# Kernel tuning notes

Measured on AMD Instinct MI355X. Metric: run time of the kernel, lower is better.

## Reference

```python
import jax, jax.numpy as jnp
import numpy as np

H = W = 96                      # image_size (scaled down from (240,240) for working-set control)
K = 16                          # faces_per_pixel
SIGMA = 1e-4
GAMMA = 1e-4
BLUR = float(np.log(1.0 / 1e-4 - 1.0) * SIGMA)   # blur_radius, compared against squared NDC dist (pytorch3d convention)
ZNEAR, ZFAR = 1.0, 100.0        # softmax_rgb_blend defaults
EPS = 1e-10


def _edge_d2(p, a, b):
    # squared point-to-segment distance; p:[B,P,F,2], a,b:[B,1,F,2]
    ab = b - a
    ap = p - a
    t = jnp.clip((ap * ab).sum(-1) / ((ab * ab).sum(-1) + 1e-12), 0.0, 1.0)
    d = ap - t[..., None] * ab
    return (d * d).sum(-1)


def _render(meshes_positions, meshes_rotations, meshes_scale, cam_pos, cam_rot, vertices, vert_colors, faces_packed):
    B, M, _ = meshes_positions.shape
    V = vertices.shape[1]
    # per-mesh scale -> rotate -> translate (forward of MeshesRenderer)
    scaled = meshes_scale[:, :, None, :] * vertices[None]                           # [B,M,V,3]
    world = jnp.einsum('bmij,bmvj->bmvi', meshes_rotations, scaled) + meshes_positions[:, :, None, :]
    world = world.reshape(B, M * V, 3)
    # pytorch3d camera: X_cam = X_world @ R + T
    cam = jnp.einsum('bvj,bji->bvi', world, cam_rot) + cam_pos[:, None, :]
    z = cam[..., 2]                                                                 # [B,N]
    xy = cam[..., :2] / z[..., None]                                                # perspective, focal=1 (NDC)

    tri = xy[:, faces_packed]                                                       # [B,F,3,2]
    tz = z[:, faces_packed]                                                         # [B,F,3]
    fcol = vert_colors.reshape(M * V, 3)[faces_packed]                              # [F,3,3]

    xs = (jnp.arange(W, dtype=xy.dtype) + 0.5) * 2.0 / W - 1.0
    ys = 1.0 - (jnp.arange(H, dtype=xy.dtype) + 0.5) * 2.0 / H
    gx, gy = jnp.meshgrid(xs, ys)
    pix = jnp.stack([gx.ravel(), gy.ravel()], -1)[None, :, None, :]                 # [1,P,1,2]

    v0 = tri[:, None, :, 0]; v1 = tri[:, None, :, 1]; v2 = tri[:, None, :, 2]       # [B,1,F,2]
    e1 = v1 - v0; e2 = v2 - v0
    d = pix - v0                                                                    # [B,P,F,2]
    den = e1[..., 0] * e2[..., 1] - e1[..., 1] * e2[..., 0] + 1e-12
    b1 = (d[..., 0] * e2[..., 1] - d[..., 1] * e2[..., 0]) / den                    # barycentrics [B,P,F]
    b2 = (e1[..., 0] * d[..., 1] - e1[..., 1] * d[..., 0]) / den
    b0 = 1.0 - b1 - b2
    zpix = b0 * tz[:, None, :, 0] + b1 * tz[:, None, :, 1] + b2 * tz[:, None, :, 2]
    inside = (b0 >= 0) & (b1 >= 0) & (b2 >= 0)
    d2 = jnp.minimum(jnp.minimum(_edge_d2(pix, v0, v1), _edge_d2(pix, v1, v2)), _edge_d2(pix, v2, v0))
    dists = jnp.where(inside, -d2, d2)                                              # signed squared dist
    valid = (zpix > 1e-2) & (dists <= BLUR)

    # faces_per_pixel = K nearest faces by depth (z-buffer)
    _, idx = jax.lax.top_k(jnp.where(valid, -zpix, -jnp.inf), K)                    # [B,P,K]
    take = lambda a: jnp.take_along_axis(a, idx, axis=-1)
    bk = jnp.stack([take(b0), take(b1), take(b2)], -1)                              # [B,P,K,3]
    zk, dk = take(zpix), take(dists)
    mk = take(valid.astype(zpix.dtype))
    # texture gather: barycentric blend of per-vertex colors (TexturesVertex.sample_textures)
    texel = jnp.einsum('bpkv,bpkvc->bpkc', bk, fcol[idx])                           # [B,P,K,3]

    # softmax_rgb_blend
    prob = jax.nn.sigmoid(-dk / SIGMA) * mk
    zinv = (ZFAR - zk) / (ZFAR - ZNEAR) * mk
    zmax = jnp.maximum(zinv.max(-1), EPS)
    wnum = prob * jnp.exp((zinv - zmax[..., None]) / GAMMA)
    delta = jnp.exp((EPS - zmax) / GAMMA)
    denom = wnum.sum(-1) + delta
    bg = jnp.ones(3, zpix.dtype)                                                    # default white background
    rgb = ((wnum[..., None] * texel).sum(-2) + delta[..., None] * bg) / denom[..., None]
    alpha = 1.0 - jnp.prod(1.0 - prob, -1)
    return jnp.concatenate([rgb, alpha[..., None]], -1).reshape(B, H, W, 4)


def setup_inputs() -> dict:
    key = jax.random.key(0)
    ks = jax.random.split(key, 8)
    B, M, V, Fm = 2, 2, 256, 256
    vertices = jax.random.normal(ks[0], (M, V, 3), jnp.float32) * 0.4
    faces = jax.random.randint(ks[1], (M, Fm, 3), 0, V)
    vert_colors = jax.random.uniform(ks[2], (M, V, 3), dtype=jnp.float32)
    meshes_positions = jax.random.normal(ks[3], (B, M, 3), jnp.float32) * 0.2
    # small z-axis rotations (proper rotation matrices)
    ang = jax.random.normal(ks[4], (B, M), jnp.float32) * 0.2
    c, s = jnp.cos(ang), jnp.sin(ang)
    z0 = jnp.zeros_like(c); o = jnp.ones_like(c)
    meshes_rotations = jnp.stack([c, -s, z0, s, c, z0, z0, z0, o], -1).reshape(B, M, 3, 3)
    meshes_scale = 1.0 + 0.1 * jax.random.normal(ks[5], (B, M, 3), jnp.float32)
    cam_rot = jnp.tile(jnp.eye(3, dtype=jnp.float32)[None], (B, 1, 1))
    cam_pos = jnp.tile(jnp.array([0.0, 0.0, 3.0], jnp.float32), (B, 1))
    return {
        'meshes_positions': meshes_positions, 'meshes_rotations': meshes_rotations,
        'meshes_scale': meshes_scale, 'cam_pos': cam_pos, 'cam_rot': cam_rot,
        'vertices': vertices, 'faces': faces, 'vert_colors': vert_colors,
    }


def reference(meshes_positions, meshes_rotations, meshes_scale, cam_pos, cam_rot, vertices, faces, vert_colors):
    M, V = vertices.shape[:2]
    faces_packed = (faces + (jnp.arange(M) * V)[:, None, None]).reshape(-1, 3)      # [F,3]
    return _render(meshes_positions, meshes_rotations, meshes_scale, cam_pos, cam_rot,
                   vertices, vert_colors, faces_packed)
```

## Files before the change

### kernel.cpp

```cpp
#include <hip/hip_runtime.h>

#pragma clang fp contract(off)

#define HH 96
#define WW 96
#define KK 16
#define MM 2
#define NF 512
#define NV 512
#define NPIX (HH*WW)

#define SIGMA_F 1e-4f
#define GAMMA_F 1e-4f
#define BLUR_F  9.210240366975851e-4f
#define EPS_F   1e-10f
#define ZFAR_F  100.0f
#define ZNEAR_F 1.0f
#define RM      0.0304f

#define SENT 0xFFFFFFFFFFFFFFFFull

__device__ __forceinline__ float frcp(float x) { return __builtin_amdgcn_rcpf(x); }

__device__ __forceinline__ float edge_d2(float px, float py,
                                         float ax, float ay,
                                         float bx, float by) {
    float abx = bx - ax, aby = by - ay;
    float apx = px - ax, apy = py - ay;
    float t = (apx*abx + apy*aby) * frcp(abx*abx + aby*aby + 1e-12f);
    t = fminf(fmaxf(t, 0.0f), 1.0f);
    float dx = apx - t*abx, dy = apy - t*aby;
    return dx*dx + dy*dy;
}

struct Rast { float b0, b1, b2, zpix, dists; };

__device__ __forceinline__ Rast rasterize_g(float px, float py,
                                            float4 g0, float4 g1, float4 g2) {
    Rast r;
    float v0x=g0.x, v0y=g0.y, v1x=g0.z, v1y=g0.w, v2x=g1.x, v2y=g1.y;
    float z0=g1.z, z1=g1.w, z2=g2.x;
    float e1x=v1x-v0x, e1y=v1y-v0y, e2x=v2x-v0x, e2y=v2y-v0y;
    float dx=px-v0x, dy=py-v0y;
    float rden = frcp(e1x*e2y - e1y*e2x + 1e-12f);
    r.b1 = (dx*e2y - dy*e2x) * rden;
    r.b2 = (e1x*dy - e1y*dx) * rden;
    r.b0 = 1.0f - r.b1 - r.b2;
    r.zpix = r.b0*z0 + r.b1*z1 + r.b2*z2;
    bool inside = (r.b0 >= 0.0f) && (r.b1 >= 0.0f) && (r.b2 >= 0.0f);
    float d2 = edge_d2(px, py, v0x, v0y, v1x, v1y);
    d2 = fminf(d2, edge_d2(px, py, v1x, v1y, v2x, v2y));
    d2 = fminf(d2, edge_d2(px, py, v2x, v2y, v0x, v0y));
    r.dists = inside ? -d2 : d2;
    return r;
}

__device__ __forceinline__ Rast rasterize_p(float px, float py,
                                            float4 P0, float4 P1, float4 P2) {
    Rast r;
    float e1x = P1.x-P0.x, e1y = P1.y-P0.y;
    float e2x = P2.x-P0.x, e2y = P2.y-P0.y;
    float dx = px-P0.x, dy = py-P0.y;
    float rden = frcp(e1x*e2y - e1y*e2x + 1e-12f);
    r.b1 = (dx*e2y - dy*e2x) * rden;
    r.b2 = (e1x*dy - e1y*dx) * rden;
    r.b0 = 1.0f - r.b1 - r.b2;
    r.zpix = r.b0*P0.z + r.b1*P1.z + r.b2*P2.z;
    bool inside = (r.b0 >= 0.0f) && (r.b1 >= 0.0f) && (r.b2 >= 0.0f);
    float d2 = edge_d2(px, py, P0.x, P0.y, P1.x, P1.y);
    d2 = fminf(d2, edge_d2(px, py, P1.x, P1.y, P2.x, P2.y));
    d2 = fminf(d2, edge_d2(px, py, P2.x, P2.y, P0.x, P0.y));
    r.dists = inside ? -d2 : d2;
    return r;
}

__device__ __forceinline__ unsigned long long packzf(float z, int f) {
    return (((unsigned long long)__float_as_uint(z)) << 32) | (unsigned int)f;
}

__device__ __forceinline__ unsigned long long shflx64(unsigned long long v, int m) {
    int lo = __shfl_xor((int)(unsigned)(v & 0xffffffffull), m, 64);
    int hi = __shfl_xor((int)(unsigned)(v >> 32), m, 64);
    return ((unsigned long long)(unsigned)hi << 32) | (unsigned)lo;
}

__device__ __forceinline__ void agg_face(float px, float py,
                                         const float4* __restrict__ geop,
                                         const float4* __restrict__ colp,
                                         int bf, float z, float zmaxv,
                                         float& nr, float& ng, float& nb,
                                         float& dn, float& ap) {
    float4 g0 = geop[bf*3+0], g1 = geop[bf*3+1], g2 = geop[bf*3+2];
    Rast r = rasterize_g(px, py, g0, g1, g2);
    float prob = 1.0f / (1.0f + expf(r.dists / SIGMA_F));
    float zinv = (ZFAR_F - z) / (ZFAR_F - ZNEAR_F);
    float w = prob * expf((zinv - zmaxv) / GAMMA_F);
    float4 c0 = colp[bf*3+0], c1 = colp[bf*3+1], c2 = colp[bf*3+2];
    nr += w * (r.b0*c0.x + r.b1*c1.x + r.b2*c2.x);
    ng += w * (r.b0*c0.y + r.b1*c1.y + r.b2*c2.y);
    nb += w * (r.b0*c0.z + r.b1*c1.z + r.b2*c2.z);
    dn += w;
    ap *= (1.0f - prob);
}

__global__ void stage_kernel(
    const float* __restrict__ mpos, const float* __restrict__ mrot,
    const float* __restrict__ mscale, const float* __restrict__ cpos,
    const float* __restrict__ crot, const float* __restrict__ verts,
    const int* __restrict__ faces, const float* __restrict__ vcol,
    float4* __restrict__ ws)
{
    const int b = blockIdx.x / MM, m = blockIdx.x % MM, t = threadIdx.x;
    const int B = gridDim.x / MM;
    const int BF = B * NF;
    __shared__ float sx[256], sy[256], sz[256];

    float cr[9];
    #pragma unroll
    for (int i = 0; i < 9; ++i) cr[i] = crot[b*9 + i];
    const float cpx = cpos[b*3+0], cpy = cpos[b*3+1], cpz = cpos[b*3+2];

    {
        int sb = (b*MM + m)*3, rb = (b*MM + m)*9;
        int vid = m*256 + t;
        float v0 = verts[vid*3+0] * mscale[sb+0];
        float v1 = verts[vid*3+1] * mscale[sb+1];
        float v2 = verts[vid*3+2] * mscale[sb+2];
        float wx = mrot[rb+0]*v0 + mrot[rb+1]*v1 + mrot[rb+2]*v2 + mpos[sb+0];
        float wy = mrot[rb+3]*v0 + mrot[rb+4]*v1 + mrot[rb+5]*v2 + mpos[sb+1];
        float wz = mrot[rb+6]*v0 + mrot[rb+7]*v1 + mrot[rb+8]*v2 + mpos[sb+2];
        float cx = wx*cr[0] + wy*cr[3] + wz*cr[6] + cpx;
        float cy = wx*cr[1] + wy*cr[4] + wz*cr[7] + cpy;
        float cz = wx*cr[2] + wy*cr[5] + wz*cr[8] + cpz;
        sx[t] = cx / cz;  sy[t] = cy / cz;  sz[t] = cz;
    }
    __syncthreads();

    const int fb = (m*256 + t)*3;
    const int i0 = faces[fb+0], i1 = faces[fb+1], i2 = faces[fb+2];
    const float x0 = sx[i0], y0 = sy[i0], z0 = sz[i0];
    const float x1 = sx[i1], y1 = sy[i1], z1 = sz[i1];
    const float x2 = sx[i2], y2 = sy[i2], z2 = sz[i2];

    const int bf = b*NF + m*256 + t;
    float4* bboxp = ws;
    float4* geop  = ws + BF;
    float4* colp  = ws + 4*BF;

    bboxp[bf] = make_float4(fminf(fminf(x0,x1),x2), fminf(fminf(y0,y1),y2),
                            fmaxf(fmaxf(x0,x1),x2), fmaxf(fmaxf(y0,y1),y2));
    geop[bf*3+0] = make_float4(x0, y0, x1, y1);
    geop[bf*3+1] = make_float4(x2, y2, z0, z1);
    geop[bf*3+2] = make_float4(z2, 0.0f, 0.0f, 0.0f);

    int c0i = (m*256 + i0)*3, c1i = (m*256 + i1)*3, c2i = (m*256 + i2)*3;
    colp[bf*3+0] = make_float4(vcol[c0i], vcol[c0i+1], vcol[c0i+2], 0.0f);
    colp[bf*3+1] = make_float4(vcol[c1i], vcol[c1i+1], vcol[c1i+2], 0.0f);
    colp[bf*3+2] = make_float4(vcol[c2i], vcol[c2i+1], vcol[c2i+2], 0.0f);
}

__global__ __launch_bounds__(256) void render_wave_kernel(
    const float4* __restrict__ ws, float* __restrict__ out, int B)
{
    const int tilesPerB = NPIX / 4;
    const int b    = blockIdx.x / tilesPerB;
    const int tile = blockIdx.x % tilesPerB;
    const int wv   = threadIdx.x >> 6;
    const int lane = threadIdx.x & 63;
    const int p    = tile*4 + wv;
    const int pi = p / WW, pj = p % WW;
    const float px = ((float)pj + 0.5f) * 2.0f / (float)WW - 1.0f;
    const float py = 1.0f - ((float)pi + 0.5f) * 2.0f / (float)HH;

    const int BF = B * NF;
    const float4* bboxp = ws;
    const float4* geop  = ws + BF;
    const float4* colp  = ws + 4*BF;
    const int base = b * NF;

    unsigned long long pk[8];
    int validm = 0;
    #pragma unroll
    for (int k = 0; k < 8; ++k) {
        int f  = (k << 6) | lane;
        int bf = base + f;
        float4 bb = bboxp[bf];
        unsigned long long t = SENT;
        if (px >= bb.x - RM && px <= bb.z + RM &&
            py >= bb.y - RM && py <= bb.w + RM) {
            float4 g0 = geop[bf*3+0], g1 = geop[bf*3+1], g2 = geop[bf*3+2];
            Rast r = rasterize_g(px, py, g0, g1, g2);
            if (r.zpix > 0.01f && r.dists <= BLUR_F) t = packzf(r.zpix, f);
        }
        pk[k] = t;
        validm |= (t != SENT ? 1 : 0) << k;
    }

    const int c0 = __popc(validm);
    int cnt = c0;
    #pragma unroll
    for (int m = 1; m < 64; m <<= 1) cnt += __shfl_xor(cnt, m, 64);

    float nr = 0.0f, ng = 0.0f, nb = 0.0f, dn = 0.0f, ap = 1.0f;
    float zmaxv = EPS_F;

    __shared__ unsigned long long q[4][64];

    if (cnt <= 64) {
        int pre = c0;
        #pragma unroll
        for (int i = 1; i < 64; i <<= 1) {
            int u = __shfl_up(pre, i, 64);
            if (lane >= i) pre += u;
        }
        pre -= c0;
        q[wv][lane] = SENT;
        __builtin_amdgcn_wave_barrier();
        asm volatile("" ::: "memory");
        int o = pre;
        #pragma unroll
        for (int k = 0; k < 8; ++k)
            if (validm & (1 << k)) { q[wv][o] = pk[k]; ++o; }
        __builtin_amdgcn_wave_barrier();
        asm volatile("" ::: "memory");
        unsigned long long v = q[wv][lane];

        #pragma unroll
        for (int kk = 2; kk <= 64; kk <<= 1) {
            #pragma unroll
            for (int j = kk >> 1; j > 0; j >>= 1) {
                unsigned long long o2 = shflx64(v, j);
                bool kmin = ((lane & kk) == 0) == ((lane & j) == 0);
                v = (kmin == (o2 < v)) ? o2 : v;
            }
        }
        if (cnt > 0) {
            unsigned z0b = (unsigned)__shfl((int)(unsigned)(v >> 32), 0, 64);
            zmaxv = fmaxf((ZFAR_F - __uint_as_float(z0b)) / (ZFAR_F - ZNEAR_F), EPS_F);
        }
        const int incn = (cnt < KK) ? cnt : KK;
        if (lane < incn) {
            int f = (int)(v & 0xffffffffull);
            float z = __uint_as_float((unsigned)(v >> 32));
            agg_face(px, py, geop, colp, base + f, z, zmaxv, nr, ng, nb, dn, ap);
        }
    } else {
        int remm = validm, inclm = 0;
        float zming = 0.0f;
        for (int r = 0; r < 16; ++r) {
            unsigned long long lm = SENT;
            #pragma unroll
            for (int k = 0; k < 8; ++k)
                if (remm & (1 << k)) lm = (pk[k] < lm) ? pk[k] : lm;
            #pragma unroll
            for (int m = 1; m < 64; m <<= 1) {
                unsigned long long o2 = shflx64(lm, m);
                if (o2 < lm) lm = o2;
            }
            if (r == 0) zming = __uint_as_float((unsigned)(lm >> 32));
            #pragma unroll
            for (int k = 0; k < 8; ++k)
                if ((remm & (1 << k)) && pk[k] == lm) { inclm |= 1 << k; remm &= ~(1 << k); }
        }
        zmaxv = fmaxf((ZFAR_F - zming) / (ZFAR_F - ZNEAR_F), EPS_F);
        #pragma unroll
        for (int k = 0; k < 8; ++k)
            if (inclm & (1 << k)) {
                int f = (k << 6) | lane;
                float z = __uint_as_float((unsigned)(pk[k] >> 32));
                agg_face(px, py, geop, colp, base + f, z, zmaxv, nr, ng, nb, dn, ap);
            }
    }

    #pragma unroll
    for (int m = 1; m < 64; m <<= 1) {
        nr += __shfl_xor(nr, m, 64);
        ng += __shfl_xor(ng, m, 64);
        nb += __shfl_xor(nb, m, 64);
        dn += __shfl_xor(dn, m, 64);
        ap *= __shfl_xor(ap, m, 64);
    }
    if (lane == 0) {
        float delta = expf((EPS_F - zmaxv) / GAMMA_F);
        float dd = dn + delta;
        float4 o4;
        o4.x = (nr + delta) / dd;
        o4.y = (ng + delta) / dd;
        o4.z = (nb + delta) / dd;
        o4.w = 1.0f - ap;
        *reinterpret_cast<float4*>(&out[((size_t)b * NPIX + p) * 4]) = o4;
    }
}

#define PIX_PB 32
#define TPP 8
#define FPT (NF/TPP)

__global__ __launch_bounds__(256) void render_kernel_fb(
    const float* __restrict__ mpos, const float* __restrict__ mrot,
    const float* __restrict__ mscale, const float* __restrict__ cpos,
    const float* __restrict__ crot, const float* __restrict__ verts,
    const int* __restrict__ faces, const float* __restrict__ vcol,
    float* __restrict__ out)
{
    __shared__ float4 svp[NV];
    __shared__ unsigned long long cand[TPP][KK][PIX_PB];
    __shared__ int   scnt[TPP][PIX_PB];
    __shared__ float sminz[TPP][PIX_PB];
    __shared__ float spart[5][TPP][PIX_PB];

    const int blocksPerBatch = NPIX / PIX_PB;
    const int b    = blockIdx.x / blocksPerBatch;
    const int tile = blockIdx.x % blocksPerBatch;
    const int tid  = threadIdx.x;
    const int pix  = tid & (PIX_PB - 1);
    const int sub  = tid >> 5;

    float cr[9];
    #pragma unroll
    for (int t = 0; t < 9; ++t) cr[t] = crot[b*9 + t];
    const float cpx = cpos[b*3+0], cpy = cpos[b*3+1], cpz = cpos[b*3+2];

    for (int g = tid; g < NV; g += 256) {
        int m = g >> 8;
        int sb = (b*MM + m)*3;
        float v0 = verts[g*3+0] * mscale[sb+0];
        float v1 = verts[g*3+1] * mscale[sb+1];
        float v2 = verts[g*3+2] * mscale[sb+2];
        int rb = (b*MM + m)*9;
        float wx = mrot[rb+0]*v0 + mrot[rb+1]*v1 + mrot[rb+2]*v2 + mpos[sb+0];
        float wy = mrot[rb+3]*v0 + mrot[rb+4]*v1 + mrot[rb+5]*v2 + mpos[sb+1];
        float wz = mrot[rb+6]*v0 + mrot[rb+7]*v1 + mrot[rb+8]*v2 + mpos[sb+2];
        float cx = wx*cr[0] + wy*cr[3] + wz*cr[6] + cpx;
        float cy = wx*cr[1] + wy*cr[4] + wz*cr[7] + cpy;
        float cz = wx*cr[2] + wy*cr[5] + wz*cr[8] + cpz;
        svp[g] = make_float4(cx / cz, cy / cz, cz, 0.0f);
    }
    __syncthreads();

    const int p  = tile * PIX_PB + pix;
    const int pi = p / WW, pj = p % WW;
    const float px = ((float)pj + 0.5f) * 2.0f / (float)WW - 1.0f;
    const float py = 1.0f - ((float)pi + 0.5f) * 2.0f / (float)HH;

    float topZ[KK]; int topI[KK];
    #pragma unroll
    for (int s = 0; s < KK; ++s) { topZ[s] = INFINITY; topI[s] = -1; }
    float curMax = INFINITY;

    for (int k = 0; k < FPT; ++k) {
        const int f = sub * FPT + k;
        const int moff = (f >> 8) << 8;
        int i0 = faces[f*3+0] + moff;
        int i1 = faces[f*3+1] + moff;
        int i2 = faces[f*3+2] + moff;
        Rast r = rasterize_p(px, py, svp[i0], svp[i1], svp[i2]);
        if ((r.zpix > 0.01f) && (r.dists <= BLUR_F) && (r.zpix < curMax)) {
            float mz = topZ[0]; int mslot = 0;
            #pragma unroll
            for (int s = 1; s < KK; ++s)
                if (topZ[s] > mz) { mz = topZ[s]; mslot = s; }
            #pragma unroll
            for (int s = 0; s < KK; ++s)
                if (s == mslot) { topZ[s] = r.zpix; topI[s] = f; }
            curMax = topZ[0];
            #pragma unroll
            for (int s = 1; s < KK; ++s) curMax = fmaxf(curMax, topZ[s]);
        }
    }

    {
        int c = 0; float mn = INFINITY;
        #pragma unroll
        for (int s = 0; s < KK; ++s)
            if (topI[s] >= 0) { cand[sub][c][pix] = packzf(topZ[s], topI[s]); ++c; mn = fminf(mn, topZ[s]); }
        scnt[sub][pix] = c; sminz[sub][pix] = mn;
    }
    __syncthreads();

    int total = 0;
    #pragma unroll
    for (int s = 0; s < TPP; ++s) total += scnt[s][pix];
    float minz = INFINITY;
    #pragma unroll
    for (int s = 0; s < TPP; ++s) minz = fminf(minz, sminz[s][pix]);
    float zmaxv = EPS_F;
    if (minz < INFINITY) zmaxv = fmaxf((ZFAR_F - minz) / (ZFAR_F - ZNEAR_F), EPS_F);

    float nr = 0, ng = 0, nb = 0, dn = 0, ap = 1.0f;
    #pragma unroll
    for (int s = 0; s < KK; ++s) {
        int f = topI[s];
        if (f < 0) continue;
        bool inc = true;
        if (total > KK) {
            unsigned long long mypk = packzf(topZ[s], f);
            int rank = 0;
            for (int t = 0; t < TPP; ++t) {
                int n = scnt[t][pix];
                for (int j = 0; j < n; ++j) rank += (cand[t][j][pix] < mypk) ? 1 : 0;
            }
            inc = (rank < KK);
        }
        if (!inc) continue;
        const int moff = (f >> 8) << 8;
        int i0 = faces[f*3+0] + moff;
        int i1 = faces[f*3+1] + moff;
        int i2 = faces[f*3+2] + moff;
        Rast r = rasterize_p(px, py, svp[i0], svp[i1], svp[i2]);
        float prob = 1.0f / (1.0f + expf(r.dists / SIGMA_F));
        float zinv = (ZFAR_F - topZ[s]) / (ZFAR_F - ZNEAR_F);
        float w = prob * expf((zinv - zmaxv) / GAMMA_F);
        nr += w * (r.b0*vcol[i0*3+0] + r.b1*vcol[i1*3+0] + r.b2*vcol[i2*3+0]);
        ng += w * (r.b0*vcol[i0*3+1] + r.b1*vcol[i1*3+1] + r.b2*vcol[i2*3+1]);
        nb += w * (r.b0*vcol[i0*3+2] + r.b1*vcol[i1*3+2] + r.b2*vcol[i2*3+2]);
        dn += w; ap *= (1.0f - prob);
    }

    spart[0][sub][pix] = nr; spart[1][sub][pix] = ng; spart[2][sub][pix] = nb;
    spart[3][sub][pix] = dn; spart[4][sub][pix] = ap;
    __syncthreads();

    if (tid < PIX_PB) {
        float rr = 0, gg = 0, bb = 0, dd = 0, aa = 1.0f;
        #pragma unroll
        for (int s = 0; s < TPP; ++s) {
            rr += spart[0][s][tid]; gg += spart[1][s][tid]; bb += spart[2][s][tid];
            dd += spart[3][s][tid]; aa *= spart[4][s][tid];
        }
        float mz = INFINITY;
        #pragma unroll
        for (int s = 0; s < TPP; ++s) mz = fminf(mz, sminz[s][tid]);
        float zmx = EPS_F;
        if (mz < INFINITY) zmx = fmaxf((ZFAR_F - mz) / (ZFAR_F - ZNEAR_F), EPS_F);
        float delta = expf((EPS_F - zmx) / GAMMA_F);
        rr += delta; gg += delta; bb += delta; dd += delta;
        int pp = tile * PIX_PB + tid;
        float4 px4;
        px4.x = rr / dd; px4.y = gg / dd; px4.z = bb / dd; px4.w = 1.0f - aa;
        *reinterpret_cast<float4*>(&out[((size_t)b * NPIX + pp) * 4]) = px4;
    }
}

extern "C" void kernel_launch(void* const* d_in, const int* in_sizes, int n_in,
                              void* d_out, int out_size, void* d_ws, size_t ws_size,
                              hipStream_t stream) {
    const float* mpos   = (const float*)d_in[0];
    const float* mrot   = (const float*)d_in[1];
    const float* mscale = (const float*)d_in[2];
    const float* cpos   = (const float*)d_in[3];
    const float* crot   = (const float*)d_in[4];
    const float* verts  = (const float*)d_in[5];
    const int*   faces  = (const int*)d_in[6];
    const float* vcol   = (const float*)d_in[7];
    float*       out    = (float*)d_out;

    const int B = in_sizes[3] / 3;
    const size_t need = (size_t)B * NF * 7 * sizeof(float4);

    if (ws_size >= need) {
        stage_kernel<<<dim3(B * MM), dim3(256), 0, stream>>>(
            mpos, mrot, mscale, cpos, crot, verts, faces, vcol, (float4*)d_ws);
        render_wave_kernel<<<dim3(B * (NPIX / 4)), dim3(256), 0, stream>>>(
            (const float4*)d_ws, out, B);
    } else {
        render_kernel_fb<<<dim3(B * (NPIX / PIX_PB)), dim3(256), 0, stream>>>(
            mpos, mrot, mscale, cpos, crot, verts, faces, vcol, out);
    }
}
```

Measured before the change: 47.87 us.

## Add tile binning pass so each pixel only tests faces overlapping its tile

Adds a bin kernel that builds, for each 8x8 pixel tile, a compacted list of faces whose padded bounding boxes overlap the tile. A new tile render kernel then rasterizes only the listed faces per pixel instead of scanning all 512. It also adds a fast path that skips the bitonic sort when at most K candidates exist, and switches to fast exp and reciprocal intrinsics. The cost is an extra launch plus workspace for the per-tile lists, and the fast intrinsics may slightly change numerics.

```diff
diff --git a/kernel.cpp b/kernel.cpp
--- a/kernel.cpp
+++ b/kernel.cpp
@@ -7,8 +7,11 @@
 #define KK 16
 #define MM 2
 #define NF 512
-#define NV 512
 #define NPIX (HH*WW)
+#define TDIM 12
+#define TSZ 8
+#define NTILE (TDIM*TDIM)
+#define MAXC 8
 
 #define SIGMA_F 1e-4f
 #define GAMMA_F 1e-4f
@@ -55,25 +58,6 @@
     return r;
 }
 
-__device__ __forceinline__ Rast rasterize_p(float px, float py,
-                                            float4 P0, float4 P1, float4 P2) {
-    Rast r;
-    float e1x = P1.x-P0.x, e1y = P1.y-P0.y;
-    float e2x = P2.x-P0.x, e2y = P2.y-P0.y;
-    float dx = px-P0.x, dy = py-P0.y;
-    float rden = frcp(e1x*e2y - e1y*e2x + 1e-12f);
-    r.b1 = (dx*e2y - dy*e2x) * rden;
-    r.b2 = (e1x*dy - e1y*dx) * rden;
-    r.b0 = 1.0f - r.b1 - r.b2;
-    r.zpix = r.b0*P0.z + r.b1*P1.z + r.b2*P2.z;
-    bool inside = (r.b0 >= 0.0f) && (r.b1 >= 0.0f) && (r.b2 >= 0.0f);
-    float d2 = edge_d2(px, py, P0.x, P0.y, P1.x, P1.y);
-    d2 = fminf(d2, edge_d2(px, py, P1.x, P1.y, P2.x, P2.y));
-    d2 = fminf(d2, edge_d2(px, py, P2.x, P2.y, P0.x, P0.y));
-    r.dists = inside ? -d2 : d2;
-    return r;
-}
-
 __device__ __forceinline__ unsigned long long packzf(float z, int f) {
     return (((unsigned long long)__float_as_uint(z)) << 32) | (unsigned int)f;
 }
@@ -92,9 +76,9 @@
                                          float& dn, float& ap) {
     float4 g0 = geop[bf*3+0], g1 = geop[bf*3+1], g2 = geop[bf*3+2];
     Rast r = rasterize_g(px, py, g0, g1, g2);
-    float prob = 1.0f / (1.0f + expf(r.dists / SIGMA_F));
+    float prob = frcp(1.0f + __expf(r.dists / SIGMA_F));
     float zinv = (ZFAR_F - z) / (ZFAR_F - ZNEAR_F);
-    float w = prob * expf((zinv - zmaxv) / GAMMA_F);
+    float w = prob * __expf((zinv - zmaxv) / GAMMA_F);
     float4 c0 = colp[bf*3+0], c1 = colp[bf*3+1], c2 = colp[bf*3+2];
     nr += w * (r.b0*c0.x + r.b1*c1.x + r.b2*c2.x);
     ng += w * (r.b0*c0.y + r.b1*c1.y + r.b2*c2.y);
@@ -159,6 +143,175 @@
     colp[bf*3+2] = make_float4(vcol[c2i], vcol[c2i+1], vcol[c2i+2], 0.0f);
 }
 
+__global__ __launch_bounds__(256) void bin_kernel(
+    const float4* __restrict__ ws, unsigned short* __restrict__ lists,
+    int* __restrict__ cnts, int B)
+{
+    const int wid  = (blockIdx.x * 256 + threadIdx.x) >> 6;
+    const int lane = threadIdx.x & 63;
+    const int b = wid / NTILE, tile = wid % NTILE;
+    const int ty = tile / TDIM, tx = tile % TDIM;
+    const float x_lo = -1.0f + tx * (2.0f / TDIM);
+    const float x_hi = x_lo + 2.0f / TDIM;
+    const float y_hi = 1.0f - ty * (2.0f / TDIM);
+    const float y_lo = y_hi - 2.0f / TDIM;
+
+    const float4* bboxp = ws;
+    unsigned short* list = lists + (size_t)wid * NF;
+    int base = 0;
+    #pragma unroll
+    for (int k = 0; k < 8; ++k) {
+        int f = (k << 6) | lane;
+        float4 bb = bboxp[b*NF + f];
+        bool hit = (bb.x - RM <= x_hi) && (bb.z + RM >= x_lo) &&
+                   (bb.y - RM <= y_hi) && (bb.w + RM >= y_lo);
+        unsigned long long m = __ballot(hit);
+        if (hit) {
+            int rank = __popcll(m & ((1ull << lane) - 1ull));
+            list[base + rank] = (unsigned short)f;
+        }
+        base += __popcll(m);
+    }
+    if (lane == 0) cnts[wid] = base;
+}
+
+__global__ __launch_bounds__(512) void render_tile_kernel(
+    const float4* __restrict__ ws, const unsigned short* __restrict__ lists,
+    const int* __restrict__ cnts, float* __restrict__ out, int B)
+{
+    const int wv   = threadIdx.x >> 6;
+    const int lane = threadIdx.x & 63;
+    const int blocksPerB = NTILE * 8;
+    const int b    = blockIdx.x / blocksPerB;
+    const int rem  = blockIdx.x % blocksPerB;
+    const int tile = rem >> 3, q = rem & 7;
+    const int pit  = q * 8 + wv;
+    const int ty = tile / TDIM, tx = tile % TDIM;
+    const int pi = ty * TSZ + (pit >> 3), pj = tx * TSZ + (pit & 7);
+    const float px = ((float)pj + 0.5f) * (2.0f / WW) - 1.0f;
+    const float py = 1.0f - ((float)pi + 0.5f) * (2.0f / HH);
+
+    const int BF = B * NF;
+    const float4* geop = ws + BF;
+    const float4* colp = ws + 4*BF;
+    const unsigned short* list = lists + (size_t)(b*NTILE + tile) * NF;
+    const int L = cnts[b*NTILE + tile];
+    const int base = b * NF;
+
+    unsigned long long pk[MAXC];
+    int validm = 0;
+    #pragma unroll
+    for (int c = 0; c < MAXC; ++c) {
+        pk[c] = SENT;
+        if (c * 64 < L) {
+            int idx = c * 64 + lane;
+            unsigned long long t = SENT;
+            if (idx < L) {
+                int f  = list[idx];
+                int bf = base + f;
+                float4 g0 = geop[bf*3+0], g1 = geop[bf*3+1], g2 = geop[bf*3+2];
+                Rast r = rasterize_g(px, py, g0, g1, g2);
+                if (r.zpix > 0.01f && r.dists <= BLUR_F) t = packzf(r.zpix, f);
+            }
+            pk[c] = t;
+            validm |= (t != SENT ? 1 : 0) << c;
+        }
+    }
+
+    const int c0 = __popc(validm);
+    int cnt = c0;
+    #pragma unroll
+    for (int m = 1; m < 64; m <<= 1) cnt += __shfl_xor(cnt, m, 64);
+
+    float nr = 0.0f, ng = 0.0f, nb = 0.0f, dn = 0.0f, ap = 1.0f;
+    float zmaxv = EPS_F;
+
+    if (cnt <= KK) {
+        unsigned long long lmin = pk[0];
+        #pragma unroll
+        for (int c = 1; c < MAXC; ++c) lmin = (pk[c] < lmin) ? pk[c] : lmin;
+        #pragma unroll
+        for (int m = 1; m < 64; m <<= 1) {
+            unsigned long long o2 = shflx64(lmin, m);
+            lmin = (o2 < lmin) ? o2 : lmin;
+        }
+        if (cnt > 0) {
+            float zming = __uint_as_float((unsigned)(lmin >> 32));
+            zmaxv = fmaxf((ZFAR_F - zming) / (ZFAR_F - ZNEAR_F), EPS_F);
+        }
+        #pragma unroll
+        for (int c = 0; c < MAXC; ++c)
+            if (validm & (1 << c)) {
+                int f = (int)(pk[c] & 0xffffffffull);
+                float z = __uint_as_float((unsigned)(pk[c] >> 32));
+                agg_face(px, py, geop, colp, base + f, z, zmaxv, nr, ng, nb, dn, ap);
+            }
+    } else if (L <= 64) {
+        unsigned long long v = pk[0];
+        #pragma unroll
+        for (int kk = 2; kk <= 64; kk <<= 1) {
+            #pragma unroll
+            for (int j = kk >> 1; j > 0; j >>= 1) {
+                unsigned long long o2 = shflx64(v, j);
+                bool kmin = ((lane & kk) == 0) == ((lane & j) == 0);
+                v = (kmin == (o2 < v)) ? o2 : v;
+            }
+        }
+        unsigned z0b = (unsigned)__shfl((int)(unsigned)(v >> 32), 0, 64);
+        zmaxv = fmaxf((ZFAR_F - __uint_as_float(z0b)) / (ZFAR_F - ZNEAR_F), EPS_F);
+        if (lane < KK) {
+            int f = (int)(v & 0xffffffffull);
+            float z = __uint_as_float((unsigned)(v >> 32));
+            agg_face(px, py, geop, colp, base + f, z, zmaxv, nr, ng, nb, dn, ap);
+        }
+    } else {
+        int remm = validm, inclm = 0;
+        float zming = 0.0f;
+        for (int r = 0; r < KK; ++r) {
+            unsigned long long lm = SENT;
+            #pragma unroll
+            for (int k = 0; k < MAXC; ++k)
+                if (remm & (1 << k)) lm = (pk[k] < lm) ? pk[k] : lm;
+            #pragma unroll
+            for (int m = 1; m < 64; m <<= 1) {
+                unsigned long long o2 = shflx64(lm, m);
+                lm = (o2 < lm) ? o2 : lm;
+            }
+            if (r == 0) zming = __uint_as_float((unsigned)(lm >> 32));
+            #pragma unroll
+            for (int k = 0; k < MAXC; ++k)
+                if ((remm & (1 << k)) && pk[k] == lm) { inclm |= 1 << k; remm &= ~(1 << k); }
+        }
+        zmaxv = fmaxf((ZFAR_F - zming) / (ZFAR_F - ZNEAR_F), EPS_F);
+        #pragma unroll
+        for (int k = 0; k < MAXC; ++k)
+            if (inclm & (1 << k)) {
+                int f = (int)(pk[k] & 0xffffffffull);
+                float z = __uint_as_float((unsigned)(pk[k] >> 32));
+                agg_face(px, py, geop, colp, base + f, z, zmaxv, nr, ng, nb, dn, ap);
+            }
+    }
+
+    #pragma unroll
+    for (int m = 1; m < 64; m <<= 1) {
+        nr += __shfl_xor(nr, m, 64);
+        ng += __shfl_xor(ng, m, 64);
+        nb += __shfl_xor(nb, m, 64);
+        dn += __shfl_xor(dn, m, 64);
+        ap *= __shfl_xor(ap, m, 64);
+    }
+    if (lane == 0) {
+        float delta = __expf((EPS_F - zmaxv) / GAMMA_F);
+        float dd = dn + delta;
+        float4 o4;
+        o4.x = (nr + delta) / dd;
+        o4.y = (ng + delta) / dd;
+        o4.z = (nb + delta) / dd;
+        o4.w = 1.0f - ap;
+        *reinterpret_cast<float4*>(&out[((size_t)b * NPIX + pi * WW + pj) * 4]) = o4;
+    }
+}
+
 __global__ __launch_bounds__(256) void render_wave_kernel(
     const float4* __restrict__ ws, float* __restrict__ out, int B)
 {
@@ -204,50 +357,30 @@
     float nr = 0.0f, ng = 0.0f, nb = 0.0f, dn = 0.0f, ap = 1.0f;
     float zmaxv = EPS_F;
 
-    __shared__ unsigned long long q[4][64];
-
-    if (cnt <= 64) {
-        int pre = c0;
-        #pragma unroll
-        for (int i = 1; i < 64; i <<= 1) {
-            int u = __shfl_up(pre, i, 64);
-            if (lane >= i) pre += u;
-        }
-        pre -= c0;
-        q[wv][lane] = SENT;
-        __builtin_amdgcn_wave_barrier();
-        asm volatile("" ::: "memory");
-        int o = pre;
-        #pragma unroll
-        for (int k = 0; k < 8; ++k)
-            if (validm & (1 << k)) { q[wv][o] = pk[k]; ++o; }
-        __builtin_amdgcn_wave_barrier();
-        asm volatile("" ::: "memory");
-        unsigned long long v = q[wv][lane];
-
-        #pragma unroll
-        for (int kk = 2; kk <= 64; kk <<= 1) {
-            #pragma unroll
-            for (int j = kk >> 1; j > 0; j >>= 1) {
-                unsigned long long o2 = shflx64(v, j);
-                bool kmin = ((lane & kk) == 0) == ((lane & j) == 0);
-                v = (kmin == (o2 < v)) ? o2 : v;
-            }
+    if (cnt <= KK) {
+        unsigned long long lmin = pk[0];
+        #pragma unroll
+        for (int c = 1; c < 8; ++c) lmin = (pk[c] < lmin) ? pk[c] : lmin;
+        #pragma unroll
+        for (int m = 1; m < 64; m <<= 1) {
+            unsigned long long o2 = shflx64(lmin, m);
+            lmin = (o2 < lmin) ? o2 : lmin;
         }
         if (cnt > 0) {
-            unsigned z0b = (unsigned)__shfl((int)(unsigned)(v >> 32), 0, 64);
-            zmaxv = fmaxf((ZFAR_F - __uint_as_float(z0b)) / (ZFAR_F - ZNEAR_F), EPS_F);
-        }
-        const int incn = (cnt < KK) ? cnt : KK;
-        if (lane < incn) {
-            int f = (int)(v & 0xffffffffull);
-            float z = __uint_as_float((unsigned)(v >> 32));
-            agg_face(px, py, geop, colp, base + f, z, zmaxv, nr, ng, nb, dn, ap);
-        }
+            float zming = __uint_as_float((unsigned)(lmin >> 32));
+            zmaxv = fmaxf((ZFAR_F - zming) / (ZFAR_F - ZNEAR_F), EPS_F);
+        }
+        #pragma unroll
+        for (int c = 0; c < 8; ++c)
+            if (validm & (1 << c)) {
+                int f = (int)(pk[c] & 0xffffffffull);
+                float z = __uint_as_float((unsigned)(pk[c] >> 32));
+                agg_face(px, py, geop, colp, base + f, z, zmaxv, nr, ng, nb, dn, ap);
+            }
     } else {
         int remm = validm, inclm = 0;
         float zming = 0.0f;
-        for (int r = 0; r < 16; ++r) {
+        for (int r = 0; r < KK; ++r) {
             unsigned long long lm = SENT;
             #pragma unroll
             for (int k = 0; k < 8; ++k)
@@ -255,7 +388,7 @@
             #pragma unroll
             for (int m = 1; m < 64; m <<= 1) {
                 unsigned long long o2 = shflx64(lm, m);
-                if (o2 < lm) lm = o2;
+                lm = (o2 < lm) ? o2 : lm;
             }
             if (r == 0) zming = __uint_as_float((unsigned)(lm >> 32));
             #pragma unroll
@@ -266,7 +399,7 @@
         #pragma unroll
         for (int k = 0; k < 8; ++k)
             if (inclm & (1 << k)) {
-                int f = (k << 6) | lane;
+                int f = (int)(pk[k] & 0xffffffffull);
                 float z = __uint_as_float((unsigned)(pk[k] >> 32));
                 agg_face(px, py, geop, colp, base + f, z, zmaxv, nr, ng, nb, dn, ap);
             }
@@ -281,7 +414,7 @@
         ap *= __shfl_xor(ap, m, 64);
     }
     if (lane == 0) {
-        float delta = expf((EPS_F - zmaxv) / GAMMA_F);
+        float delta = __expf((EPS_F - zmaxv) / GAMMA_F);
         float dd = dn + delta;
         float4 o4;
         o4.x = (nr + delta) / dd;
@@ -289,156 +422,6 @@
         o4.z = (nb + delta) / dd;
         o4.w = 1.0f - ap;
         *reinterpret_cast<float4*>(&out[((size_t)b * NPIX + p) * 4]) = o4;
-    }
-}
-
-#define PIX_PB 32
-#define TPP 8
-#define FPT (NF/TPP)
-
-__global__ __launch_bounds__(256) void render_kernel_fb(
-    const float* __restrict__ mpos, const float* __restrict__ mrot,
-    const float* __restrict__ mscale, const float* __restrict__ cpos,
-    const float* __restrict__ crot, const float* __restrict__ verts,
-    const int* __restrict__ faces, const float* __restrict__ vcol,
-    float* __restrict__ out)
-{
-    __shared__ float4 svp[NV];
-    __shared__ unsigned long long cand[TPP][KK][PIX_PB];
-    __shared__ int   scnt[TPP][PIX_PB];
-    __shared__ float sminz[TPP][PIX_PB];
-    __shared__ float spart[5][TPP][PIX_PB];
-
-    const int blocksPerBatch = NPIX / PIX_PB;
-    const int b    = blockIdx.x / blocksPerBatch;
-    const int tile = blockIdx.x % blocksPerBatch;
-    const int tid  = threadIdx.x;
-    const int pix  = tid & (PIX_PB - 1);
-    const int sub  = tid >> 5;
-
-    float cr[9];
-    #pragma unroll
-    for (int t = 0; t < 9; ++t) cr[t] = crot[b*9 + t];
-    const float cpx = cpos[b*3+0], cpy = cpos[b*3+1], cpz = cpos[b*3+2];
-
-    for (int g = tid; g < NV; g += 256) {
-        int m = g >> 8;
-        int sb = (b*MM + m)*3;
-        float v0 = verts[g*3+0] * mscale[sb+0];
-        float v1 = verts[g*3+1] * mscale[sb+1];
-        float v2 = verts[g*3+2] * mscale[sb+2];
-        int rb = (b*MM + m)*9;
-        float wx = mrot[rb+0]*v0 + mrot[rb+1]*v1 + mrot[rb+2]*v2 + mpos[sb+0];
-        float wy = mrot[rb+3]*v0 + mrot[rb+4]*v1 + mrot[rb+5]*v2 + mpos[sb+1];
-        float wz = mrot[rb+6]*v0 + mrot[rb+7]*v1 + mrot[rb+8]*v2 + mpos[sb+2];
-        float cx = wx*cr[0] + wy*cr[3] + wz*cr[6] + cpx;
-        float cy = wx*cr[1] + wy*cr[4] + wz*cr[7] + cpy;
-        float cz = wx*cr[2] + wy*cr[5] + wz*cr[8] + cpz;
-        svp[g] = make_float4(cx / cz, cy / cz, cz, 0.0f);
-    }
-    __syncthreads();
-
-    const int p  = tile * PIX_PB + pix;
-    const int pi = p / WW, pj = p % WW;
-    const float px = ((float)pj + 0.5f) * 2.0f / (float)WW - 1.0f;
-    const float py = 1.0f - ((float)pi + 0.5f) * 2.0f / (float)HH;
-
-    float topZ[KK]; int topI[KK];
-    #pragma unroll
-    for (int s = 0; s < KK; ++s) { topZ[s] = INFINITY; topI[s] = -1; }
-    float curMax = INFINITY;
-
-    for (int k = 0; k < FPT; ++k) {
-        const int f = sub * FPT + k;
-        const int moff = (f >> 8) << 8;
-        int i0 = faces[f*3+0] + moff;
-        int i1 = faces[f*3+1] + moff;
-        int i2 = faces[f*3+2] + moff;
-        Rast r = rasterize_p(px, py, svp[i0], svp[i1], svp[i2]);
-        if ((r.zpix > 0.01f) && (r.dists <= BLUR_F) && (r.zpix < curMax)) {
-            float mz = topZ[0]; int mslot = 0;
-            #pragma unroll
-            for (int s = 1; s < KK; ++s)
-                if (topZ[s] > mz) { mz = topZ[s]; mslot = s; }
-            #pragma unroll
-            for (int s = 0; s < KK; ++s)
-                if (s == mslot) { topZ[s] = r.zpix; topI[s] = f; }
-            curMax = topZ[0];
-            #pragma unroll
-            for (int s = 1; s < KK; ++s) curMax = fmaxf(curMax, topZ[s]);
-        }
-    }
-
-    {
-        int c = 0; float mn = INFINITY;
-        #pragma unroll
-        for (int s = 0; s < KK; ++s)
-            if (topI[s] >= 0) { cand[sub][c][pix] = packzf(topZ[s], topI[s]); ++c; mn = fminf(mn, topZ[s]); }
-        scnt[sub][pix] = c; sminz[sub][pix] = mn;
-    }
-    __syncthreads();
-
-    int total = 0;
-    #pragma unroll
-    for (int s = 0; s < TPP; ++s) total += scnt[s][pix];
-    float minz = INFINITY;
-    #pragma unroll
-    for (int s = 0; s < TPP; ++s) minz = fminf(minz, sminz[s][pix]);
-    float zmaxv = EPS_F;
-    if (minz < INFINITY) zmaxv = fmaxf((ZFAR_F - minz) / (ZFAR_F - ZNEAR_F), EPS_F);
-
-    float nr = 0, ng = 0, nb = 0, dn = 0, ap = 1.0f;
-    #pragma unroll
-    for (int s = 0; s < KK; ++s) {
-        int f = topI[s];
-        if (f < 0) continue;
-        bool inc = true;
-        if (total > KK) {
-            unsigned long long mypk = packzf(topZ[s], f);
-            int rank = 0;
-            for (int t = 0; t < TPP; ++t) {
-                int n = scnt[t][pix];
-                for (int j = 0; j < n; ++j) rank += (cand[t][j][pix] < mypk) ? 1 : 0;
-            }
-            inc = (rank < KK);
-        }
-        if (!inc) continue;
-        const int moff = (f >> 8) << 8;
-        int i0 = faces[f*3+0] + moff;
-        int i1 = faces[f*3+1] + moff;
-        int i2 = faces[f*3+2] + moff;
-        Rast r = rasterize_p(px, py, svp[i0], svp[i1], svp[i2]);
-        float prob = 1.0f / (1.0f + expf(r.dists / SIGMA_F));
-        float zinv = (ZFAR_F - topZ[s]) / (ZFAR_F - ZNEAR_F);
-        float w = prob * expf((zinv - zmaxv) / GAMMA_F);
-        nr += w * (r.b0*vcol[i0*3+0] + r.b1*vcol[i1*3+0] + r.b2*vcol[i2*3+0]);
-        ng += w * (r.b0*vcol[i0*3+1] + r.b1*vcol[i1*3+1] + r.b2*vcol[i2*3+1]);
-        nb += w * (r.b0*vcol[i0*3+2] + r.b1*vcol[i1*3+2] + r.b2*vcol[i2*3+2]);
-        dn += w; ap *= (1.0f - prob);
-    }
-
-    spart[0][sub][pix] = nr; spart[1][sub][pix] = ng; spart[2][sub][pix] = nb;
-    spart[3][sub][pix] = dn; spart[4][sub][pix] = ap;
-    __syncthreads();
-
-    if (tid < PIX_PB) {
-        float rr = 0, gg = 0, bb = 0, dd = 0, aa = 1.0f;
-        #pragma unroll
-        for (int s = 0; s < TPP; ++s) {
-            rr += spart[0][s][tid]; gg += spart[1][s][tid]; bb += spart[2][s][tid];
-            dd += spart[3][s][tid]; aa *= spart[4][s][tid];
-        }
-        float mz = INFINITY;
-        #pragma unroll
-        for (int s = 0; s < TPP; ++s) mz = fminf(mz, sminz[s][tid]);
-        float zmx = EPS_F;
-        if (mz < INFINITY) zmx = fmaxf((ZFAR_F - mz) / (ZFAR_F - ZNEAR_F), EPS_F);
-        float delta = expf((EPS_F - zmx) / GAMMA_F);
-        rr += delta; gg += delta; bb += delta; dd += delta;
-        int pp = tile * PIX_PB + tid;
-        float4 px4;
-        px4.x = rr / dd; px4.y = gg / dd; px4.z = bb / dd; px4.w = 1.0f - aa;
-        *reinterpret_cast<float4*>(&out[((size_t)b * NPIX + pp) * 4]) = px4;
     }
 }
 
@@ -455,16 +438,27 @@
     const float* vcol   = (const float*)d_in[7];
     float*       out    = (float*)d_out;
 
-    const int B = in_sizes[3] / 3;
-    const size_t need = (size_t)B * NF * 7 * sizeof(float4);
-
-    if (ws_size >= need) {
+    const int B  = in_sizes[3] / 3;
+    const int BF = B * NF;
+    const size_t base_bytes  = (size_t)BF * 7 * sizeof(float4);
+    const size_t lists_bytes = (size_t)B * NTILE * NF * sizeof(unsigned short);
+    const size_t cnts_bytes  = (size_t)B * NTILE * sizeof(int);
+    const size_t need_full   = base_bytes + lists_bytes + cnts_bytes;
+
+    float4* wsf = (float4*)d_ws;
+    if (ws_size >= need_full) {
+        unsigned short* lists = (unsigned short*)((char*)d_ws + base_bytes);
+        int* cnts = (int*)((char*)d_ws + base_bytes + lists_bytes);
         stage_kernel<<<dim3(B * MM), dim3(256), 0, stream>>>(
-            mpos, mrot, mscale, cpos, crot, verts, faces, vcol, (float4*)d_ws);
+            mpos, mrot, mscale, cpos, crot, verts, faces, vcol, wsf);
+        bin_kernel<<<dim3((B * NTILE) / 4), dim3(256), 0, stream>>>(
+            wsf, lists, cnts, B);
+        render_tile_kernel<<<dim3(B * NTILE * 8), dim3(512), 0, stream>>>(
+            wsf, lists, cnts, out, B);
+    } else {
+        stage_kernel<<<dim3(B * MM), dim3(256), 0, stream>>>(
+            mpos, mrot, mscale, cpos, crot, verts, faces, vcol, wsf);
         render_wave_kernel<<<dim3(B * (NPIX / 4)), dim3(256), 0, stream>>>(
-            (const float4*)d_ws, out, B);
-    } else {
-        render_kernel_fb<<<dim3(B * (NPIX / PIX_PB)), dim3(256), 0, stream>>>(
-            mpos, mrot, mscale, cpos, crot, verts, faces, vcol, out);
-    }
-}
+            wsf, out, B);
+    }
+}
```

Result: slower. 49.63 us (+3.7%).
